# Kernel tuning notes

Hardware: AMD Instinct MI355X
Metric: run time of the kernel (lower is better)

Reference implementation:

```python
import jax, jax.numpy as jnp
import numpy as np

B, N, T, FH, H = 4, 5000, 12, 12, 128
DEG = 16
BN = B * N


def setup_inputs():
    key = jax.random.key(0)
    ks = jax.random.split(key, 12)
    rng = np.random.default_rng(0)
    e = N * DEG
    s = rng.integers(0, N, size=(B, e))
    d = rng.integers(0, N, size=(B, e))
    off = (np.arange(B) * N)[:, None]
    edge_index = jnp.asarray(np.stack([(s + off).ravel(), (d + off).ravel()]), dtype=jnp.int32)

    def lin(k, i, o):
        return jax.random.normal(k, (i, o), jnp.float32) / np.sqrt(i).astype(np.float32)

    return {
        "x": jax.random.normal(ks[0], (B, N, T), jnp.float32),
        "gcn_w1": lin(ks[1], 1, 64), "gcn_b1": jnp.zeros(64),
        "gcn_w2": lin(ks[2], 64, H), "gcn_b2": jnp.zeros(H),
        "gcn_w3": lin(ks[3], H, H), "gcn_b3": jnp.zeros(H),
        "att_w1": lin(ks[4], H, H), "att_b1": jnp.zeros(H),
        "att_w2": lin(ks[5], H, 1), "att_b2": jnp.zeros(1),
        "gru_w_ih": jax.random.normal(ks[6], (3 * H, H), jnp.float32) / np.sqrt(H).astype(np.float32),
        "gru_w_hh": jax.random.normal(ks[7], (3 * H, H), jnp.float32) / np.sqrt(H).astype(np.float32),
        "gru_b_ih": jnp.zeros(3 * H), "gru_b_hh": jnp.zeros(3 * H),
        "ode_w1": lin(ks[8], H, H), "ode_b1": jnp.zeros(H),
        "ode_w2": lin(ks[9], H, H), "ode_b2": jnp.zeros(H),
        "out_w": lin(ks[10], H, 1), "out_b": jnp.zeros(1),
        "edge_index": edge_index,
    }


def _forward(x, gcn_w1, gcn_b1, gcn_w2, gcn_b2, gcn_w3, gcn_b3,
             att_w1, att_b1, att_w2, att_b2,
             gru_w_ih, gru_w_hh, gru_b_ih, gru_b_hh,
             ode_w1, ode_b1, ode_w2, ode_b2, out_w, out_b, edge_index):
    # GCNConv with added self-loops and symmetric normalization (PyG semantics)
    loops = jnp.arange(BN, dtype=edge_index.dtype)
    src = jnp.concatenate([edge_index[0], loops])
    dst = jnp.concatenate([edge_index[1], loops])
    deg = jnp.zeros(BN, x.dtype).at[dst].add(1.0)  # >= 1 thanks to self-loops
    dinv = jax.lax.rsqrt(deg)
    norm = (dinv[src] * dinv[dst])[:, None]  # (E+BN, 1)

    def gcn(h, W, b):
        h = h @ W  # (BN, out)
        agg = jnp.zeros((BN, W.shape[1]), h.dtype).at[dst].add(h[src] * norm)
        return agg + b

    # spatial encoder per timestep (scan over the small time axis)
    x_steps = x.reshape(BN, T).T[:, :, None]  # (T, BN, 1)

    def spatial_step(_, x_t):
        h = jax.nn.relu(gcn(x_t, gcn_w1, gcn_b1))
        h = jax.nn.relu(gcn(h, gcn_w2, gcn_b2))
        h = jax.nn.relu(gcn(h, gcn_w3, gcn_b3))
        return None, h

    _, h_seq = jax.lax.scan(spatial_step, None, x_steps)  # (T, BN, H)
    h_seq = h_seq.reshape(T, B, N, H).transpose(1, 0, 2, 3)  # (B, T, N, H)

    # temporal attention over time axis
    att = jnp.tanh(h_seq @ att_w1 + att_b1) @ att_w2 + att_b2  # (B, T, N, 1)
    aw = jax.nn.softmax(att, axis=1)
    node_features = jnp.sum(h_seq * aw, axis=1).reshape(BN, H)

    # single-step GRU with zero initial hidden (torch gate order r, z, n)
    h0 = jnp.zeros((BN, H), x.dtype)
    gi = node_features @ gru_w_ih.T + gru_b_ih
    gh = h0 @ gru_w_hh.T + gru_b_hh
    ir, iz, inn = jnp.split(gi, 3, axis=1)
    hr, hz, hn = jnp.split(gh, 3, axis=1)
    r = jax.nn.sigmoid(ir + hr)
    z = jax.nn.sigmoid(iz + hz)
    n = jnp.tanh(inn + r * hn)
    hidden = (1.0 - z) * n + z * h0  # (BN, H)

    # Graph ODE: dh/dt = tanh(GCN(tanh(GCN(h)))), RK4 on t=linspace(0,FH,FH)
    def ode_f(h):
        h = jnp.tanh(gcn(h, ode_w1, ode_b1))
        return jnp.tanh(gcn(h, ode_w2, ode_b2))

    dt = FH / (FH - 1)

    def rk4(h, _):
        k1 = ode_f(h)
        k2 = ode_f(h + 0.5 * dt * k1)
        k3 = ode_f(h + 0.5 * dt * k2)
        k4 = ode_f(h + dt * k3)
        h2 = h + (dt / 6.0) * (k1 + 2.0 * k2 + 2.0 * k3 + k4)
        return h2, h2

    _, traj = jax.lax.scan(rk4, hidden, None, length=FH - 1)
    states = jnp.concatenate([hidden[None], traj], axis=0)  # (FH, BN, H)
    ev = states.reshape(FH, B, N, H).transpose(1, 2, 0, 3)  # (B, N, FH, H)
    return (ev @ out_w + out_b)[..., 0]  # (B, N, FH)


def reference(x, gcn_w1, gcn_b1, gcn_w2, gcn_b2, gcn_w3, gcn_b3,
              att_w1, att_b1, att_w2, att_b2,
              gru_w_ih, gru_w_hh, gru_b_ih, gru_b_hh,
              ode_w1, ode_b1, ode_w2, ode_b2, out_w, out_b, edge_index):
    return _forward(x, gcn_w1, gcn_b1, gcn_w2, gcn_b2, gcn_w3, gcn_b3,
                    att_w1, att_b1, att_w2, att_b2,
                    gru_w_ih, gru_w_hh, gru_b_ih, gru_b_hh,
                    ode_w1, ode_b1, ode_w2, ode_b2, out_w, out_b, edge_index)
```

## Files before the change

### kernel.cpp

```cpp
#include <hip/hip_runtime.h>
#include <stdint.h>

#define B_ 4
#define N_ 5000
#define T_ 12
#define FH_ 12
#define H_ 128
#define BN_ 20000
#define E_ 320000
#define TOTE_ (E_ + BN_)
#define EVCAP_ (TOTE_ + BN_)
#define EDCAP_ 190000
#define NTB_ 313
#define NT_ 1252
#define SLOTB_ 5008
#define BNS_ 20032
#define DCAP_ 512

typedef __attribute__((ext_vector_type(8))) short s8v;
typedef __attribute__((ext_vector_type(4))) float f32x4;

__device__ __forceinline__ float fast_tanh(float x) {
  float e = __expf(2.f * x);
  return 1.f - 2.f * __builtin_amdgcn_rcpf(e + 1.f);
}
__device__ __forceinline__ float fast_sigmoid(float x) {
  return __builtin_amdgcn_rcpf(1.f + __expf(-x));
}
__device__ __forceinline__ unsigned short f2bf(float f) {
  unsigned u = __float_as_uint(f);
  u = (u + 0x7fffu + ((u >> 16) & 1u)) >> 16;
  return (unsigned short)u;
}
__device__ __forceinline__ float bf2f(unsigned short u) {
  return __uint_as_float(((unsigned)u) << 16);
}
__device__ __forceinline__ unsigned pack2(float lo, float hi) {
  return ((unsigned)f2bf(hi) << 16) | f2bf(lo);
}
#define DOT2ACC(accv, pa, pb, sel)                                         \
  {                                                                        \
    unsigned pp_ = __builtin_amdgcn_perm((pb), (pa), (sel));               \
    asm("v_dot2_f32_bf16 %0, %1, %2, %0" : "+v"(accv) : "v"(pp_), "v"(wp)); \
  }

__global__ void k_sentinel(float* out) { out[0] = 1e30f; }

__global__ void k_init_cnt(int* cnt) {
  int i = blockIdx.x * 256 + threadIdx.x;
  if (i < BN_) cnt[i] = 1;
}
__global__ void k_count(const int* __restrict__ dst, int* cnt) {
  int e = blockIdx.x * 256 + threadIdx.x;
  if (e < E_) atomicAdd(&cnt[dst[e]], 1);
}
__global__ void k_scan(int* cnt, int* rp, float* dinv) {
  __shared__ int sh[1024];
  int tid = threadIdx.x;
  const int per = (BN_ + 1023) / 1024;
  int start = tid * per;
  int end = start + per; if (end > BN_) end = BN_;
  int s = 0;
  for (int i = start; i < end; i++) {
    int c = cnt[i];
    dinv[i] = rsqrtf((float)c);
    s += (c + 1) & ~1;
  }
  sh[tid] = s;
  __syncthreads();
  for (int off = 1; off < 1024; off <<= 1) {
    int v = (tid >= off) ? sh[tid - off] : 0;
    __syncthreads();
    sh[tid] += v;
    __syncthreads();
  }
  int run = (tid > 0) ? sh[tid - 1] : 0;
  for (int i = start; i < end; i++) {
    int c = cnt[i];
    rp[i] = run;
    run += (c + 1) & ~1;
    cnt[i] = 0;
  }
  if (tid == 1023) rp[BN_] = sh[1023];
}
__global__ void k_fill(const int* __restrict__ src, const int* __restrict__ dst,
                       const int* __restrict__ rp, int* cnt, int2* ev,
                       const float* __restrict__ dinv) {
  int e = blockIdx.x * 256 + threadIdx.x;
  if (e >= TOTE_) return;
  int s, d;
  if (e < E_) { s = src[e]; d = dst[e]; }
  else { s = d = e - E_; }
  int pos = rp[d] + atomicAdd(&cnt[d], 1);
  int2 p; p.x = s * 128; p.y = __float_as_int(dinv[s] * dinv[d]);
  ev[pos] = p;
}

__global__ void k_hist(const int* __restrict__ rp, int* hist) {
  int i = blockIdx.x * 256 + threadIdx.x;
  if (i < BN_) {
    int d = (rp[i + 1] - rp[i]) >> 1; d = d > 63 ? 63 : d;
    atomicAdd(&hist[(i / N_) * 64 + (63 - d)], 1);
  }
}
__global__ void k_binscan(int* hist) {
  __shared__ int sh[256];
  int t = threadIdx.x;
  int val = hist[t];
  sh[t] = val;
  __syncthreads();
  for (int o = 1; o < 256; o <<= 1) {
    int v = (t >= o) ? sh[t - o] : 0;
    __syncthreads();
    sh[t] += v;
    __syncthreads();
  }
  hist[t] = sh[t] - val;
}
__global__ void k_scatter(const int* __restrict__ rp, int* hist, int* ord, int* posj) {
  int i = blockIdx.x * 256 + threadIdx.x;
  if (i < BN_) {
    int d = (rp[i + 1] - rp[i]) >> 1; d = d > 63 ? 63 : d;
    int gpos = atomicAdd(&hist[(i / N_) * 64 + (63 - d)], 1);
    ord[gpos] = i;
    posj[i] = gpos - (i / N_) * N_;
  }
}

__global__ void k_rowoff(const int* __restrict__ rp, const int* __restrict__ ord,
                         int* rowoffp, int* tcntp) {
  int t = blockIdx.x * 256 + threadIdx.x;
  if (t >= NT_) return;
  int bb = t / NTB_, within = t % NTB_;
  int acc = 0;
  for (int r = 0; r < 16; r++) {
    int j = within * 16 + r;
    int plen = 0;
    if (j < N_) {
      int row = ord[bb * N_ + j];
      plen = (rp[row + 1] - rp[row]) >> 1;
    }
    rowoffp[t * 16 + r] = acc;
    acc += plen;
  }
  tcntp[t] = acc;
}
__global__ void k_tscan(const int* __restrict__ tcnt, int* __restrict__ tstart) {
  __shared__ int sh[1024];
  int tid = threadIdx.x;
  int st = tid * 2, en = st + 2; if (en > NT_) en = NT_;
  int s = 0;
  for (int i = st; i < en; i++) s += tcnt[i];
  sh[tid] = s;
  __syncthreads();
  for (int o = 1; o < 1024; o <<= 1) {
    int v = (tid >= o) ? sh[tid - o] : 0;
    __syncthreads();
    sh[tid] += v;
    __syncthreads();
  }
  int run = tid ? sh[tid - 1] : 0;
  for (int i = st; i < en; i++) { tstart[i] = run; run += tcnt[i]; }
  if (tid == 1023) tstart[NT_] = sh[1023];
}
__global__ void k_edfill(const int* __restrict__ rp, const int* __restrict__ ord,
                         const int* __restrict__ posj, const int2* __restrict__ ev,
                         const int* __restrict__ tstartp, const int* __restrict__ rowoffp,
                         int2* __restrict__ ed) {
  int idx = blockIdx.x * 256 + threadIdx.x;
  if (idx >= NT_ * 16) return;
  int t = idx >> 4, r = idx & 15;
  int bb = t / NTB_, within = t % NTB_;
  int j = within * 16 + r;
  if (j >= N_) return;
  int row = ord[bb * N_ + j];
  int b0 = rp[row], len = rp[row + 1] - b0;
  int dst = tstartp[t] + rowoffp[t * 16 + r];
  for (int i = 0; i < len; i += 2) {
    int2 pA = ev[b0 + i], pB = ev[b0 + i + 1];
    int sA = pA.x >> 7, sB = pB.x >> 7;
    int slotA = (sA / N_) * SLOTB_ + posj[sA];
    int slotB = (sB / N_) * SLOTB_ + posj[sB];
    unsigned wp = ((unsigned)f2bf(__int_as_float(pB.y)) << 16) |
                  f2bf(__int_as_float(pA.y));
    int2 o; o.x = slotA | (slotB << 16); o.y = (int)wp;
    ed[dst + (i >> 1)] = o;
  }
}

__device__ __forceinline__ void prep_one(const float* __restrict__ src,
                                         unsigned short* __restrict__ dst,
                                         int K, int Nn, int transposed, int idx) {
  int j = idx & 7, l = (idx >> 3) & 63, rest = idx >> 9;
  int NT = Nn >> 4;
  int nt = rest % NT, kc = rest / NT;
  int k = kc * 32 + ((l >> 4) << 3) + j;
  int n = nt * 16 + (l & 15);
  float v = transposed ? src[n * K + k] : src[k * Nn + n];
  dst[idx] = f2bf(v);
}
__global__ void k_prep_all(const float* w2, const float* w3, const float* a1,
                           const float* o1, const float* o2, const float* wih,
                           unsigned short* w2f, unsigned short* w3f, unsigned short* a1f,
                           unsigned short* o1f, unsigned short* o2f, unsigned short* wihf) {
  int idx = blockIdx.x * 256 + threadIdx.x;
  if (idx < 8192) { prep_one(w2, w2f, 64, 128, 0, idx); return; }
  idx -= 8192;
  if (idx < 16384) { prep_one(w3, w3f, 128, 128, 0, idx); return; }
  idx -= 16384;
  if (idx < 16384) { prep_one(a1, a1f, 128, 128, 0, idx); return; }
  idx -= 16384;
  if (idx < 16384) { prep_one(o1, o1f, 128, 128, 0, idx); return; }
  idx -= 16384;
  if (idx < 16384) { prep_one(o2, o2f, 128, 128, 0, idx); return; }
  idx -= 16384;
  if (idx < 49152) prep_one(wih, wihf, 128, 384, 1, idx);
}

__global__ void k_spl1T(const int* __restrict__ rp, const int2* __restrict__ ev,
                        const int* __restrict__ posj,
                        const float* __restrict__ x,
                        const float* __restrict__ w1, const float* __restrict__ b1,
                        unsigned short* __restrict__ h1) {
  int wid = (blockIdx.x * 256 + threadIdx.x) >> 6;
  int lane = threadIdx.x & 63;
  if (wid >= BN_) return;
  int beg = rp[wid], end = rp[wid + 1];
  float a[12];
#pragma unroll
  for (int t = 0; t < 12; t++) a[t] = 0.f;
  for (int e = beg + lane; e < end; e += 64) {
    int2 p = ev[e];
    const float4* xp = (const float4*)(x + (size_t)(p.x >> 7) * 12);
    float v = __int_as_float(p.y);
    float4 x0 = xp[0], x1 = xp[1], x2 = xp[2];
    a[0] = fmaf(v, x0.x, a[0]);  a[1] = fmaf(v, x0.y, a[1]);
    a[2] = fmaf(v, x0.z, a[2]);  a[3] = fmaf(v, x0.w, a[3]);
    a[4] = fmaf(v, x1.x, a[4]);  a[5] = fmaf(v, x1.y, a[5]);
    a[6] = fmaf(v, x1.z, a[6]);  a[7] = fmaf(v, x1.w, a[7]);
    a[8] = fmaf(v, x2.x, a[8]);  a[9] = fmaf(v, x2.y, a[9]);
    a[10] = fmaf(v, x2.z, a[10]); a[11] = fmaf(v, x2.w, a[11]);
  }
#pragma unroll
  for (int t = 0; t < 12; t++)
#pragma unroll
    for (int m = 1; m < 64; m <<= 1) a[t] += __shfl_xor(a[t], m);
  float wv = w1[lane], bv = b1[lane];
  int slot = (wid / N_) * SLOTB_ + posj[wid];
#pragma unroll
  for (int t = 0; t < 12; t++) {
    float v = fmaf(a[t], wv, bv);
    h1[((size_t)t * BNS_ + slot) * 64 + lane] = f2bf(fmaxf(v, 0.f));
  }
}

template<int KIN>
__device__ __forceinline__ void gather_tile(
    const int2* __restrict__ ed, const int* __restrict__ tstartp,
    const int* __restrict__ rowoffp, const unsigned short* __restrict__ in,
    unsigned short (*agg)[KIN + 8], int2* desc, int tileid, int w, int l, int tid) {
  constexpr int SH = (KIN == 128) ? 7 : 6;
  constexpr int CW = KIN / 16;
  const int h = l >> 4, c = l & 15;
  const unsigned short* inc = in + c * CW;
  int tp0 = tstartp[tileid];
  int npair = tstartp[tileid + 1] - tp0;
  if (npair > DCAP_) npair = DCAP_;
  const int2* edp = ed + tp0;
  for (int i = tid; i < npair; i += 256) desc[i] = edp[i];
  __syncthreads();
  int q0[4], qlen[4];
  float a[4][CW];
  int mx = 0;
  const int* rot = rowoffp + tileid * 16;
#pragma unroll
  for (int r = 0; r < 4; r++) {
    int lr = w * 4 + r;
    int ro = rot[lr];
    int rn = (lr == 15) ? npair : rot[lr + 1];
    int lenp = rn - ro;
    int s0 = (lenp * h) >> 2, s1 = (lenp * (h + 1)) >> 2;
    q0[r] = ro + s0;
    qlen[r] = s1 - s0;
    mx = qlen[r] > mx ? qlen[r] : mx;
#pragma unroll
    for (int q = 0; q < CW; q++) a[r][q] = 0.f;
  }
  int lim = npair - 1;
  for (int i = 0; i < mx; i++) {
#pragma unroll
    for (int r = 0; r < 4; r++) {
      int idx = q0[r] + i; idx = idx > lim ? lim : idx;
      int2 d = desc[idx];
      if (i < qlen[r]) {
        unsigned sa = (unsigned)d.x & 0xffffu;
        unsigned sb = (unsigned)d.x >> 16;
        unsigned wp = (unsigned)d.y;
        if (KIN == 128) {
          uint4 PA = *(const uint4*)(inc + ((size_t)sa << SH));
          uint4 PB = *(const uint4*)(inc + ((size_t)sb << SH));
          DOT2ACC(a[r][0], PA.x, PB.x, 0x05040100u);
          DOT2ACC(a[r][1], PA.x, PB.x, 0x07060302u);
          DOT2ACC(a[r][2], PA.y, PB.y, 0x05040100u);
          DOT2ACC(a[r][3], PA.y, PB.y, 0x07060302u);
          DOT2ACC(a[r][4], PA.z, PB.z, 0x05040100u);
          DOT2ACC(a[r][5], PA.z, PB.z, 0x07060302u);
          DOT2ACC(a[r][6], PA.w, PB.w, 0x05040100u);
          DOT2ACC(a[r][7], PA.w, PB.w, 0x07060302u);
        } else {
          uint2 PA = *(const uint2*)(inc + ((size_t)sa << SH));
          uint2 PB = *(const uint2*)(inc + ((size_t)sb << SH));
          DOT2ACC(a[r][0], PA.x, PB.x, 0x05040100u);
          DOT2ACC(a[r][1], PA.x, PB.x, 0x07060302u);
          DOT2ACC(a[r][2], PA.y, PB.y, 0x05040100u);
          DOT2ACC(a[r][3], PA.y, PB.y, 0x07060302u);
        }
      }
    }
  }
#pragma unroll
  for (int r = 0; r < 4; r++) {
#pragma unroll
    for (int q2 = 0; q2 < CW; q2++) {
      a[r][q2] += __shfl_xor(a[r][q2], 16);
      a[r][q2] += __shfl_xor(a[r][q2], 32);
    }
    if (h == 0) {
      if (KIN == 128) {
        uint4 o;
        o.x = pack2(a[r][0], a[r][1]); o.y = pack2(a[r][2], a[r][3]);
        o.z = pack2(a[r][4], a[r][5]); o.w = pack2(a[r][6], a[r][7]);
        *(uint4*)&agg[w * 4 + r][c * 8] = o;
      } else {
        uint2 o;
        o.x = pack2(a[r][0], a[r][1]); o.y = pack2(a[r][2], a[r][3]);
        *(uint2*)&agg[w * 4 + r][c * 4] = o;
      }
    }
  }
}

template<int KIN>
__device__ __forceinline__ void mfma_tile(
    const unsigned short (*agg)[KIN + 8], const unsigned short* __restrict__ Wf,
    int w, int l, f32x4 acc[2]) {
  constexpr int KC = KIN / 32;
  const int hi = l >> 4, lo16 = l & 15;
  acc[0] = (f32x4){0.f, 0.f, 0.f, 0.f};
  acc[1] = (f32x4){0.f, 0.f, 0.f, 0.f};
#pragma unroll
  for (int kc = 0; kc < KC; kc++) {
    s8v av = *(const s8v*)&agg[lo16][kc * 32 + hi * 8];
#pragma unroll
    for (int q = 0; q < 2; q++) {
      s8v bv = *(const s8v*)(Wf + (((size_t)(kc * 8 + 2 * w + q)) << 9) + (l << 3));
      acc[q] = __builtin_amdgcn_mfma_f32_16x16x32_bf16(av, bv, acc[q], 0, 0, 0);
    }
  }
}

template<int KIN>
__global__ __launch_bounds__(256) void k_fusedT(
    const int2* __restrict__ ed, const int* __restrict__ tstartp,
    const int* __restrict__ rowoffp,
    const unsigned short* __restrict__ inb, const unsigned short* __restrict__ Wf,
    const float* __restrict__ bias, unsigned short* __restrict__ outb) {
  __shared__ __align__(16) int2 desc[DCAP_];
  __shared__ unsigned short agg[16][KIN + 8];
  const int tid = threadIdx.x, l = tid & 63, w = tid >> 6;
  const int t = blockIdx.y;
  const unsigned short* in = inb + (size_t)t * BNS_ * KIN;
  unsigned short* out = outb + (size_t)t * BNS_ * 128;
  const int bid = blockIdx.x;
  const int xcd = bid & 7, slot = bid >> 3;
  const int bb = xcd >> 1;
  const int within = slot * 2 + (xcd & 1);
  if (within >= NTB_) return;
  int nv = N_ - within * 16; nv = nv > 16 ? 16 : nv;
  const int tileid = bb * NTB_ + within;
  gather_tile<KIN>(ed, tstartp, rowoffp, in, agg, desc, tileid, w, l, tid);
  __syncthreads();
  f32x4 acc[2];
  mfma_tile<KIN>(agg, Wf, w, l, acc);
  const int hi = l >> 4, lo16 = l & 15;
  const int rowbase = tileid * 16;
#pragma unroll
  for (int q = 0; q < 2; q++) {
    int col = (2 * w + q) * 16 + lo16;
    float bi = bias[col];
#pragma unroll
    for (int reg = 0; reg < 4; reg++) {
      int lr = hi * 4 + reg;
      if (lr < nv)
        out[(size_t)(rowbase + lr) * 128 + col] = f2bf(fmaxf(acc[q][reg] + bi, 0.f));
    }
  }
}

__global__ __launch_bounds__(256) void k_fused(
    const int2* __restrict__ ed, const int* __restrict__ tstartp,
    const int* __restrict__ rowoffp, const int* __restrict__ ord,
    const unsigned short* __restrict__ in,
    const unsigned short* __restrict__ Wf, const float* __restrict__ bias,
    int mode, float c1, float c2,
    unsigned short* __restrict__ outb,
    const unsigned short* __restrict__ hbfin, unsigned short* __restrict__ rkb,
    float* __restrict__ h, unsigned short* __restrict__ ubfout,
    const float* __restrict__ ow, const float* __restrict__ ob,
    float* __restrict__ outp, int step) {
  __shared__ __align__(16) int2 desc[DCAP_];
  __shared__ unsigned short agg[16][136];
  __shared__ float ppart[4][16];
  const int tid = threadIdx.x, l = tid & 63, w = tid >> 6;
  const int bid = blockIdx.x;
  const int xcd = bid & 7, slot = bid >> 3;
  const int bb = xcd >> 1;
  const int within = slot * 2 + (xcd & 1);
  if (within >= NTB_) return;
  int nv = N_ - within * 16; nv = nv > 16 ? 16 : nv;
  const int tileid = bb * NTB_ + within;
  gather_tile<128>(ed, tstartp, rowoffp, in, agg, desc, tileid, w, l, tid);
  __syncthreads();
  f32x4 acc[2];
  mfma_tile<128>(agg, Wf, w, l, acc);
  const int hi = l >> 4, lo16 = l & 15;
  const int rowbase = tileid * 16;
  float p[4] = {0.f, 0.f, 0.f, 0.f};
#pragma unroll
  for (int q = 0; q < 2; q++) {
    int col = (2 * w + q) * 16 + lo16;
    float bi = bias[col];
    float owv = (mode == 3) ? ow[col] : 0.f;
#pragma unroll
    for (int reg = 0; reg < 4; reg++) {
      int lr = hi * 4 + reg;
      if (lr >= nv) continue;
      size_t oi = (size_t)(rowbase + lr) * 128 + col;
      float v = fast_tanh(acc[q][reg] + bi);
      if (mode == 0) {
        outb[oi] = f2bf(v);
      } else if (mode == 1) {
        rkb[oi] = f2bf(v);
        ubfout[oi] = f2bf(fmaf(c1, v, bf2f(hbfin[oi])));
      } else if (mode == 2) {
        rkb[oi] = f2bf(bf2f(rkb[oi]) + 2.f * v);
        ubfout[oi] = f2bf(fmaf(c1, v, bf2f(hbfin[oi])));
      } else {
        float nh = fmaf(c2, bf2f(rkb[oi]) + v, h[oi]);
        h[oi] = nh;
        ubfout[oi] = f2bf(nh);
        p[reg] = fmaf(nh, owv, p[reg]);
      }
    }
  }
  if (mode == 3) {
#pragma unroll
    for (int m = 1; m <= 8; m <<= 1)
#pragma unroll
      for (int reg = 0; reg < 4; reg++) p[reg] += __shfl_xor(p[reg], m);
    if (lo16 == 0)
#pragma unroll
      for (int reg = 0; reg < 4; reg++) ppart[w][hi * 4 + reg] = p[reg];
    __syncthreads();
    if (tid < 16 && tid < nv) {
      int orig = ord[bb * N_ + within * 16 + tid];
      outp[(size_t)orig * FH_ + step] =
          ppart[0][tid] + ppart[1][tid] + ppart[2][tid] + ppart[3][tid] + ob[0];
    }
  }
}

__global__ __launch_bounds__(256) void k_att(
    const unsigned short* __restrict__ A, const unsigned short* __restrict__ Wf,
    const float* __restrict__ bias, int nrows,
    const float* __restrict__ w2v, const float* __restrict__ b2,
    float* __restrict__ scores) {
  const int tid = threadIdx.x;
  const int l = tid & 63;
  const int w = tid >> 6;
  const int m0 = blockIdx.x * 64 + w * 16;

  f32x4 acc[8];
#pragma unroll
  for (int nt = 0; nt < 8; nt++) acc[nt] = (f32x4){0.f, 0.f, 0.f, 0.f};
  int arow = m0 + (l & 15);
  if (arow >= nrows) arow = nrows - 1;
  const unsigned short* Ap = A + (size_t)arow * 128 + ((l >> 4) << 3);
#pragma unroll
  for (int kc = 0; kc < 4; kc++) {
    s8v av = *(const s8v*)(Ap + kc * 32);
#pragma unroll
    for (int nt = 0; nt < 8; nt++) {
      s8v bv = *(const s8v*)(Wf + (((size_t)(kc * 8 + nt)) << 9) + (l << 3));
      acc[nt] = __builtin_amdgcn_mfma_f32_16x16x32_bf16(av, bv, acc[nt], 0, 0, 0);
    }
  }
  float p[4] = {0.f, 0.f, 0.f, 0.f};
#pragma unroll
  for (int nt = 0; nt < 8; nt++) {
    int col = nt * 16 + (l & 15);
    float bi = bias[col], wv = w2v[col];
#pragma unroll
    for (int reg = 0; reg < 4; reg++)
      p[reg] = fmaf(fast_tanh(acc[nt][reg] + bi), wv, p[reg]);
  }
#pragma unroll
  for (int m = 1; m <= 8; m <<= 1)
#pragma unroll
    for (int reg = 0; reg < 4; reg++) p[reg] += __shfl_xor(p[reg], m);
  if ((l & 15) == 0) {
    float bb = b2[0];
#pragma unroll
    for (int reg = 0; reg < 4; reg++) {
      int row = m0 + ((l >> 4) << 2) + reg;
      if (row < nrows) scores[row] = p[reg] + bb;
    }
  }
}

__global__ void k_attw(const float* __restrict__ sc, const unsigned short* __restrict__ hs,
                       unsigned short* __restrict__ nf) {
  int idx = blockIdx.x * 256 + threadIdx.x;
  if (idx >= BNS_ * 64) return;
  int bn = idx >> 6, c = idx & 63;
  float v[T_];
  float m = -1e30f;
#pragma unroll
  for (int t = 0; t < T_; t++) { v[t] = sc[t * BNS_ + bn]; m = fmaxf(m, v[t]); }
  float ssum = 0.f;
#pragma unroll
  for (int t = 0; t < T_; t++) { v[t] = __expf(v[t] - m); ssum += v[t]; }
  float inv = __builtin_amdgcn_rcpf(ssum);
  float s0 = 0.f, s1 = 0.f;
#pragma unroll
  for (int t = 0; t < T_; t++) {
    unsigned p = *(const unsigned*)(hs + ((size_t)t * BNS_ + bn) * 128 + c * 2);
    float aw = v[t] * inv;
    s0 = fmaf(aw, bf2f((unsigned short)(p & 0xffffu)), s0);
    s1 = fmaf(aw, bf2f((unsigned short)(p >> 16)), s1);
  }
  *(unsigned*)(nf + (size_t)bn * 128 + c * 2) = pack2(s0, s1);
}

__global__ __launch_bounds__(256) void k_gruf(
    const unsigned short* __restrict__ A, const unsigned short* __restrict__ Wf,
    const float* __restrict__ bih, const float* __restrict__ bhh,
    const int* __restrict__ ord,
    float* __restrict__ hst, unsigned short* __restrict__ hbf,
    const float* __restrict__ ow, const float* __restrict__ ob,
    float* __restrict__ outp) {
  const int tid = threadIdx.x;
  const int l = tid & 63;
  const int w = tid >> 6;
  const int m0 = blockIdx.x * 64 + w * 16;

  f32x4 acc[24];
#pragma unroll
  for (int nt = 0; nt < 24; nt++) acc[nt] = (f32x4){0.f, 0.f, 0.f, 0.f};
  int arow = m0 + (l & 15);
  const unsigned short* Ap = A + (size_t)arow * 128 + ((l >> 4) << 3);
#pragma unroll
  for (int kc = 0; kc < 4; kc++) {
    s8v av = *(const s8v*)(Ap + kc * 32);
#pragma unroll
    for (int nt = 0; nt < 24; nt++) {
      s8v bv = *(const s8v*)(Wf + (((size_t)(kc * 24 + nt)) << 9) + (l << 3));
      acc[nt] = __builtin_amdgcn_mfma_f32_16x16x32_bf16(av, bv, acc[nt], 0, 0, 0);
    }
  }
  const int hi = l >> 4, lo16 = l & 15;
  float p[4] = {0.f, 0.f, 0.f, 0.f};
#pragma unroll
  for (int nt = 0; nt < 8; nt++) {
    int col = nt * 16 + lo16;
    float br = bih[col], bz = bih[col + 128], bn = bih[col + 256];
    float hr = bhh[col], hz = bhh[col + 128], hn = bhh[col + 256];
    float owv = ow[col];
#pragma unroll
    for (int reg = 0; reg < 4; reg++) {
      int slot = m0 + hi * 4 + reg;
      float r = fast_sigmoid(acc[nt][reg] + br + hr);
      float z = fast_sigmoid(acc[nt + 8][reg] + bz + hz);
      float n = fast_tanh(acc[nt + 16][reg] + bn + r * hn);
      float hv = (1.f - z) * n;
      size_t oi = (size_t)slot * 128 + col;
      hst[oi] = hv;
      hbf[oi] = f2bf(hv);
      p[reg] = fmaf(hv, owv, p[reg]);
    }
  }
#pragma unroll
  for (int m = 1; m <= 8; m <<= 1)
#pragma unroll
    for (int reg = 0; reg < 4; reg++) p[reg] += __shfl_xor(p[reg], m);
  if (lo16 == 0) {
    float obv = ob[0];
#pragma unroll
    for (int reg = 0; reg < 4; reg++) {
      int slot = m0 + hi * 4 + reg;
      int bbv = slot / SLOTB_;
      int j = slot - bbv * SLOTB_;
      if (j < N_) {
        int orig = ord[bbv * N_ + j];
        outp[(size_t)orig * FH_ + 0] = p[reg] + obv;
      }
    }
  }
}

extern "C" void kernel_launch(void* const* d_in, const int* in_sizes, int n_in,
                              void* d_out, int out_size, void* d_ws, size_t ws_size,
                              hipStream_t stream) {
  const float* x       = (const float*)d_in[0];
  const float* gcn_w1  = (const float*)d_in[1];
  const float* gcn_b1  = (const float*)d_in[2];
  const float* gcn_w2  = (const float*)d_in[3];
  const float* gcn_b2  = (const float*)d_in[4];
  const float* gcn_w3  = (const float*)d_in[5];
  const float* gcn_b3  = (const float*)d_in[6];
  const float* att_w1  = (const float*)d_in[7];
  const float* att_b1  = (const float*)d_in[8];
  const float* att_w2  = (const float*)d_in[9];
  const float* att_b2  = (const float*)d_in[10];
  const float* gru_wih = (const float*)d_in[11];
  const float* gru_bih = (const float*)d_in[13];
  const float* gru_bhh = (const float*)d_in[14];
  const float* ode_w1  = (const float*)d_in[15];
  const float* ode_b1  = (const float*)d_in[16];
  const float* ode_w2  = (const float*)d_in[17];
  const float* ode_b2  = (const float*)d_in[18];
  const float* out_w   = (const float*)d_in[19];
  const float* out_b   = (const float*)d_in[20];
  const int*   eidx    = (const int*)d_in[21];
  float* out = (float*)d_out;

  float* wsf = (float*)d_ws;
  size_t off = 0;
  unsigned short* h1b12 = (unsigned short*)(wsf + off); off += (size_t)12 * BNS_ * 32;
  float* hst    = wsf + off; off += (size_t)BNS_ * H_;
  float* scores = wsf + off; off += (size_t)T_ * BNS_;
  float* dinv   = wsf + off; off += BN_;
  int2*  ev     = (int2*)(wsf + off); off += (size_t)EVCAP_ * 2;
  int2*  ed     = (int2*)(wsf + off); off += (size_t)EDCAP_ * 2;
  unsigned short* hseqb  = (unsigned short*)(wsf + off); off += (size_t)T_ * BNS_ * 64;
  unsigned short* t1b12  = (unsigned short*)(wsf + off); off += (size_t)T_ * BNS_ * 64;
  unsigned short* hbf    = (unsigned short*)(wsf + off); off += (size_t)BNS_ * 64;
  unsigned short* ubf    = (unsigned short*)(wsf + off); off += (size_t)BNS_ * 64;
  unsigned short* rkb    = (unsigned short*)(wsf + off); off += (size_t)BNS_ * 64;
  unsigned short* nfbf   = (unsigned short*)(wsf + off); off += (size_t)BNS_ * 64;
  unsigned short* w2f    = (unsigned short*)(wsf + off); off += 64 * 128 / 2;
  unsigned short* w3f    = (unsigned short*)(wsf + off); off += 128 * 128 / 2;
  unsigned short* aw1f   = (unsigned short*)(wsf + off); off += 128 * 128 / 2;
  unsigned short* ow1f   = (unsigned short*)(wsf + off); off += 128 * 128 / 2;
  unsigned short* ow2f   = (unsigned short*)(wsf + off); off += 128 * 128 / 2;
  unsigned short* wihf   = (unsigned short*)(wsf + off); off += 128 * 384 / 2;
  int* rp      = (int*)(wsf + off); off += BN_ + 1;
  int* cnt     = (int*)(wsf + off); off += BN_;
  int* ord     = (int*)(wsf + off); off += BN_;
  int* posj    = (int*)(wsf + off); off += BN_;
  int* hist    = (int*)(wsf + off); off += 256;
  int* rowoffp = (int*)(wsf + off); off += (size_t)NT_ * 16;
  int* tcntp   = (int*)(wsf + off); off += NT_;
  int* tstartp = (int*)(wsf + off); off += NT_ + 1;
  if (ws_size < off * sizeof(float)) {
    k_sentinel<<<1, 1, 0, stream>>>(out);
    return;
  }

  const int* esrc = eidx;
  const int* edst = eidx + E_;
  const int g79 = (BN_ + 255) / 256;

  hipMemsetAsync(ev, 0, (size_t)EVCAP_ * sizeof(int2), stream);
  hipMemsetAsync(hist, 0, 256 * sizeof(int), stream);
  k_init_cnt<<<g79, 256, 0, stream>>>(cnt);
  k_count<<<(E_ + 255) / 256, 256, 0, stream>>>(edst, cnt);
  k_scan<<<1, 1024, 0, stream>>>(cnt, rp, dinv);
  k_fill<<<(TOTE_ + 255) / 256, 256, 0, stream>>>(esrc, edst, rp, cnt, ev, dinv);
  k_hist<<<g79, 256, 0, stream>>>(rp, hist);
  k_binscan<<<1, 256, 0, stream>>>(hist);
  k_scatter<<<g79, 256, 0, stream>>>(rp, hist, ord, posj);
  k_rowoff<<<(NT_ + 255) / 256, 256, 0, stream>>>(rp, ord, rowoffp, tcntp);
  k_tscan<<<1, 1024, 0, stream>>>(tcntp, tstartp);
  k_edfill<<<(NT_ * 16 + 255) / 256, 256, 0, stream>>>(rp, ord, posj, ev,
                                                       tstartp, rowoffp, ed);
  k_prep_all<<<480, 256, 0, stream>>>(gcn_w2, gcn_w3, att_w1, ode_w1, ode_w2, gru_wih,
                                      w2f, w3f, aw1f, ow1f, ow2f, wihf);

  const int gW = BN_ / 4;
  const int gF = 1280;

  k_spl1T<<<gW, 256, 0, stream>>>(rp, ev, posj, x, gcn_w1, gcn_b1, h1b12);
  k_fusedT<64><<<dim3(gF, 12), 256, 0, stream>>>(ed, tstartp, rowoffp,
                                                 h1b12, w2f, gcn_b2, t1b12);
  k_fusedT<128><<<dim3(gF, 12), 256, 0, stream>>>(ed, tstartp, rowoffp,
                                                  t1b12, w3f, gcn_b3, hseqb);

  k_att<<<(T_ * BNS_ + 63) / 64, 256, 0, stream>>>(hseqb, aw1f, att_b1, T_ * BNS_,
                                                   att_w2, att_b2, scores);
  k_attw<<<(BNS_ * 64 + 255) / 256, 256, 0, stream>>>(scores, hseqb, nfbf);

  k_gruf<<<BNS_ / 64, 256, 0, stream>>>(nfbf, wihf, gru_bih, gru_bhh, ord,
                                        hst, hbf, out_w, out_b, out);

  const float dt = (float)FH_ / (float)(FH_ - 1);
  unsigned short* t1 = t1b12;
  auto f_eval = [&](const unsigned short* inbf, int mode, float c1, float c2, int step) {
    k_fused<<<gF, 256, 0, stream>>>(ed, tstartp, rowoffp, ord, inbf, ow1f, ode_b1,
                                    0, 0.f, 0.f, t1, nullptr, nullptr, nullptr, nullptr,
                                    nullptr, nullptr, nullptr, 0);
    k_fused<<<gF, 256, 0, stream>>>(ed, tstartp, rowoffp, ord, t1, ow2f, ode_b2,
                                    mode, c1, c2, nullptr, hbf, rkb, hst,
                                    (mode == 3) ? hbf : ubf,
                                    out_w, out_b, out, step);
  };
  for (int s = 1; s < FH_; s++) {
    f_eval(hbf, 1, 0.5f * dt, 0.f, s);
    f_eval(ubf, 2, 0.5f * dt, 0.f, s);
    f_eval(ubf, 2, dt, 0.f, s);
    f_eval(ubf, 3, 0.f, dt / 6.f, s);
  }
}
```

Measured before the change: 1.737 ms.

## Use 8 waves per fused GCN tile block, two rows and one column tile each

Doubles the block size of the fused gather+MFMA kernels from 256 to 512 threads. Each of the 8 waves now gathers 2 of the 16 tile rows instead of 4 and computes one 16-column MFMA output tile instead of two. The mode-3 output projection reduction is widened to sum 8 partials. The aim is more memory-level parallelism and shorter per-wave serial gather loops, at the cost of more waves per tile and lower per-wave register reuse.

```diff
diff --git a/kernel.cpp b/kernel.cpp
--- a/kernel.cpp
+++ b/kernel.cpp
@@ -255,7 +255,7 @@
 }
 
 template<int KIN>
-__device__ __forceinline__ void gather_tile(
+__device__ __forceinline__ void gather_tile8(
     const int2* __restrict__ ed, const int* __restrict__ tstartp,
     const int* __restrict__ rowoffp, const unsigned short* __restrict__ in,
     unsigned short (*agg)[KIN + 8], int2* desc, int tileid, int w, int l, int tid) {
@@ -267,15 +267,15 @@
   int npair = tstartp[tileid + 1] - tp0;
   if (npair > DCAP_) npair = DCAP_;
   const int2* edp = ed + tp0;
-  for (int i = tid; i < npair; i += 256) desc[i] = edp[i];
+  for (int i = tid; i < npair; i += 512) desc[i] = edp[i];
   __syncthreads();
-  int q0[4], qlen[4];
-  float a[4][CW];
+  int q0[2], qlen[2];
+  float a[2][CW];
   int mx = 0;
   const int* rot = rowoffp + tileid * 16;
 #pragma unroll
-  for (int r = 0; r < 4; r++) {
-    int lr = w * 4 + r;
+  for (int r = 0; r < 2; r++) {
+    int lr = w * 2 + r;
     int ro = rot[lr];
     int rn = (lr == 15) ? npair : rot[lr + 1];
     int lenp = rn - ro;
@@ -286,10 +286,10 @@
 #pragma unroll
     for (int q = 0; q < CW; q++) a[r][q] = 0.f;
   }
-  int lim = npair - 1;
+  const int lim = npair - 1;
   for (int i = 0; i < mx; i++) {
 #pragma unroll
-    for (int r = 0; r < 4; r++) {
+    for (int r = 0; r < 2; r++) {
       int idx = q0[r] + i; idx = idx > lim ? lim : idx;
       int2 d = desc[idx];
       if (i < qlen[r]) {
@@ -319,7 +319,7 @@
     }
   }
 #pragma unroll
-  for (int r = 0; r < 4; r++) {
+  for (int r = 0; r < 2; r++) {
 #pragma unroll
     for (int q2 = 0; q2 < CW; q2++) {
       a[r][q2] += __shfl_xor(a[r][q2], 16);
@@ -330,37 +330,33 @@
         uint4 o;
         o.x = pack2(a[r][0], a[r][1]); o.y = pack2(a[r][2], a[r][3]);
         o.z = pack2(a[r][4], a[r][5]); o.w = pack2(a[r][6], a[r][7]);
-        *(uint4*)&agg[w * 4 + r][c * 8] = o;
+        *(uint4*)&agg[w * 2 + r][c * 8] = o;
       } else {
         uint2 o;
         o.x = pack2(a[r][0], a[r][1]); o.y = pack2(a[r][2], a[r][3]);
-        *(uint2*)&agg[w * 4 + r][c * 4] = o;
+        *(uint2*)&agg[w * 2 + r][c * 4] = o;
       }
     }
   }
 }
 
 template<int KIN>
-__device__ __forceinline__ void mfma_tile(
+__device__ __forceinline__ void mfma_tile8(
     const unsigned short (*agg)[KIN + 8], const unsigned short* __restrict__ Wf,
-    int w, int l, f32x4 acc[2]) {
+    int w, int l, f32x4& acc) {
   constexpr int KC = KIN / 32;
   const int hi = l >> 4, lo16 = l & 15;
-  acc[0] = (f32x4){0.f, 0.f, 0.f, 0.f};
-  acc[1] = (f32x4){0.f, 0.f, 0.f, 0.f};
+  acc = (f32x4){0.f, 0.f, 0.f, 0.f};
 #pragma unroll
   for (int kc = 0; kc < KC; kc++) {
     s8v av = *(const s8v*)&agg[lo16][kc * 32 + hi * 8];
-#pragma unroll
-    for (int q = 0; q < 2; q++) {
-      s8v bv = *(const s8v*)(Wf + (((size_t)(kc * 8 + 2 * w + q)) << 9) + (l << 3));
-      acc[q] = __builtin_amdgcn_mfma_f32_16x16x32_bf16(av, bv, acc[q], 0, 0, 0);
-    }
+    s8v bv = *(const s8v*)(Wf + (((size_t)(kc * 8 + w)) << 9) + (l << 3));
+    acc = __builtin_amdgcn_mfma_f32_16x16x32_bf16(av, bv, acc, 0, 0, 0);
   }
 }
 
 template<int KIN>
-__global__ __launch_bounds__(256) void k_fusedT(
+__global__ __launch_bounds__(512, 8) void k_fusedT(
     const int2* __restrict__ ed, const int* __restrict__ tstartp,
     const int* __restrict__ rowoffp,
     const unsigned short* __restrict__ inb, const unsigned short* __restrict__ Wf,
@@ -378,26 +374,23 @@
   if (within >= NTB_) return;
   int nv = N_ - within * 16; nv = nv > 16 ? 16 : nv;
   const int tileid = bb * NTB_ + within;
-  gather_tile<KIN>(ed, tstartp, rowoffp, in, agg, desc, tileid, w, l, tid);
+  gather_tile8<KIN>(ed, tstartp, rowoffp, in, agg, desc, tileid, w, l, tid);
   __syncthreads();
-  f32x4 acc[2];
-  mfma_tile<KIN>(agg, Wf, w, l, acc);
+  f32x4 acc;
+  mfma_tile8<KIN>(agg, Wf, w, l, acc);
   const int hi = l >> 4, lo16 = l & 15;
   const int rowbase = tileid * 16;
-#pragma unroll
-  for (int q = 0; q < 2; q++) {
-    int col = (2 * w + q) * 16 + lo16;
-    float bi = bias[col];
-#pragma unroll
-    for (int reg = 0; reg < 4; reg++) {
-      int lr = hi * 4 + reg;
-      if (lr < nv)
-        out[(size_t)(rowbase + lr) * 128 + col] = f2bf(fmaxf(acc[q][reg] + bi, 0.f));
-    }
-  }
-}
-
-__global__ __launch_bounds__(256) void k_fused(
+  int col = w * 16 + lo16;
+  float bi = bias[col];
+#pragma unroll
+  for (int reg = 0; reg < 4; reg++) {
+    int lr = hi * 4 + reg;
+    if (lr < nv)
+      out[(size_t)(rowbase + lr) * 128 + col] = f2bf(fmaxf(acc[reg] + bi, 0.f));
+  }
+}
+
+__global__ __launch_bounds__(512, 8) void k_fused(
     const int2* __restrict__ ed, const int* __restrict__ tstartp,
     const int* __restrict__ rowoffp, const int* __restrict__ ord,
     const unsigned short* __restrict__ in,
@@ -410,7 +403,7 @@
     float* __restrict__ outp, int step) {
   __shared__ __align__(16) int2 desc[DCAP_];
   __shared__ unsigned short agg[16][136];
-  __shared__ float ppart[4][16];
+  __shared__ float ppart[8][16];
   const int tid = threadIdx.x, l = tid & 63, w = tid >> 6;
   const int bid = blockIdx.x;
   const int xcd = bid & 7, slot = bid >> 3;
@@ -419,38 +412,35 @@
   if (within >= NTB_) return;
   int nv = N_ - within * 16; nv = nv > 16 ? 16 : nv;
   const int tileid = bb * NTB_ + within;
-  gather_tile<128>(ed, tstartp, rowoffp, in, agg, desc, tileid, w, l, tid);
+  gather_tile8<128>(ed, tstartp, rowoffp, in, agg, desc, tileid, w, l, tid);
   __syncthreads();
-  f32x4 acc[2];
-  mfma_tile<128>(agg, Wf, w, l, acc);
+  f32x4 acc;
+  mfma_tile8<128>(agg, Wf, w, l, acc);
   const int hi = l >> 4, lo16 = l & 15;
   const int rowbase = tileid * 16;
   float p[4] = {0.f, 0.f, 0.f, 0.f};
-#pragma unroll
-  for (int q = 0; q < 2; q++) {
-    int col = (2 * w + q) * 16 + lo16;
-    float bi = bias[col];
-    float owv = (mode == 3) ? ow[col] : 0.f;
-#pragma unroll
-    for (int reg = 0; reg < 4; reg++) {
-      int lr = hi * 4 + reg;
-      if (lr >= nv) continue;
-      size_t oi = (size_t)(rowbase + lr) * 128 + col;
-      float v = fast_tanh(acc[q][reg] + bi);
-      if (mode == 0) {
-        outb[oi] = f2bf(v);
-      } else if (mode == 1) {
-        rkb[oi] = f2bf(v);
-        ubfout[oi] = f2bf(fmaf(c1, v, bf2f(hbfin[oi])));
-      } else if (mode == 2) {
-        rkb[oi] = f2bf(bf2f(rkb[oi]) + 2.f * v);
-        ubfout[oi] = f2bf(fmaf(c1, v, bf2f(hbfin[oi])));
-      } else {
-        float nh = fmaf(c2, bf2f(rkb[oi]) + v, h[oi]);
-        h[oi] = nh;
-        ubfout[oi] = f2bf(nh);
-        p[reg] = fmaf(nh, owv, p[reg]);
-      }
+  int col = w * 16 + lo16;
+  float bi = bias[col];
+  float owv = (mode == 3) ? ow[col] : 0.f;
+#pragma unroll
+  for (int reg = 0; reg < 4; reg++) {
+    int lr = hi * 4 + reg;
+    if (lr >= nv) continue;
+    size_t oi = (size_t)(rowbase + lr) * 128 + col;
+    float v = fast_tanh(acc[reg] + bi);
+    if (mode == 0) {
+      outb[oi] = f2bf(v);
+    } else if (mode == 1) {
+      rkb[oi] = f2bf(v);
+      ubfout[oi] = f2bf(fmaf(c1, v, bf2f(hbfin[oi])));
+    } else if (mode == 2) {
+      rkb[oi] = f2bf(bf2f(rkb[oi]) + 2.f * v);
+      ubfout[oi] = f2bf(fmaf(c1, v, bf2f(hbfin[oi])));
+    } else {
+      float nh = fmaf(c2, bf2f(rkb[oi]) + v, h[oi]);
+      h[oi] = nh;
+      ubfout[oi] = f2bf(nh);
+      p[reg] = fmaf(nh, owv, p[reg]);
     }
   }
   if (mode == 3) {
@@ -464,8 +454,9 @@
     __syncthreads();
     if (tid < 16 && tid < nv) {
       int orig = ord[bb * N_ + within * 16 + tid];
-      outp[(size_t)orig * FH_ + step] =
-          ppart[0][tid] + ppart[1][tid] + ppart[2][tid] + ppart[3][tid] + ob[0];
+      float s = ppart[0][tid] + ppart[1][tid] + ppart[2][tid] + ppart[3][tid] +
+                ppart[4][tid] + ppart[5][tid] + ppart[6][tid] + ppart[7][tid];
+      outp[(size_t)orig * FH_ + step] = s + ob[0];
     }
   }
 }
@@ -691,9 +682,9 @@
   const int gF = 1280;
 
   k_spl1T<<<gW, 256, 0, stream>>>(rp, ev, posj, x, gcn_w1, gcn_b1, h1b12);
-  k_fusedT<64><<<dim3(gF, 12), 256, 0, stream>>>(ed, tstartp, rowoffp,
+  k_fusedT<64><<<dim3(gF, 12), 512, 0, stream>>>(ed, tstartp, rowoffp,
                                                  h1b12, w2f, gcn_b2, t1b12);
-  k_fusedT<128><<<dim3(gF, 12), 256, 0, stream>>>(ed, tstartp, rowoffp,
+  k_fusedT<128><<<dim3(gF, 12), 512, 0, stream>>>(ed, tstartp, rowoffp,
                                                   t1b12, w3f, gcn_b3, hseqb);
 
   k_att<<<(T_ * BNS_ + 63) / 64, 256, 0, stream>>>(hseqb, aw1f, att_b1, T_ * BNS_,
@@ -706,10 +697,10 @@
   const float dt = (float)FH_ / (float)(FH_ - 1);
   unsigned short* t1 = t1b12;
   auto f_eval = [&](const unsigned short* inbf, int mode, float c1, float c2, int step) {
-    k_fused<<<gF, 256, 0, stream>>>(ed, tstartp, rowoffp, ord, inbf, ow1f, ode_b1,
+    k_fused<<<gF, 512, 0, stream>>>(ed, tstartp, rowoffp, ord, inbf, ow1f, ode_b1,
                                     0, 0.f, 0.f, t1, nullptr, nullptr, nullptr, nullptr,
                                     nullptr, nullptr, nullptr, 0);
-    k_fused<<<gF, 256, 0, stream>>>(ed, tstartp, rowoffp, ord, t1, ow2f, ode_b2,
+    k_fused<<<gF, 512, 0, stream>>>(ed, tstartp, rowoffp, ord, t1, ow2f, ode_b2,
                                     mode, c1, c2, nullptr, hbf, rkb, hst,
                                     (mode == 3) ? hbf : ubf,
                                     out_w, out_b, out, step);
```

After: 1.747 ms. No clear change (+0.6%).
